# Kernel optimization log

Hardware: AMD Instinct MI355X
Metric: run time of the kernel (lower is better)

## Reference

```python
import jax, jax.numpy as jnp
import numpy as np

N = 200000          # number of points (dental scan vertices)
K = 16              # neighbors after dropping self (nsample=17 - 1)
C = 32              # feature dim (base_fdim)
NUM_CLASSES = 17
TEMPERATURE = 0.1
WEIGHT = 0.1        # head_cfg.weight[1:] of '.1'
EPS = 1e-8


def setup_inputs() -> dict:
    key = jax.random.key(0)
    k1, k2, k3 = jax.random.split(key, 3)
    features = jax.random.normal(k1, (N, C), dtype=jnp.float32)
    labels = jax.random.randint(k2, (N,), 0, NUM_CLASSES, dtype=jnp.int32)
    neighbor_idx = jax.random.randint(k3, (N, K), 0, N, dtype=jnp.int64)
    return {"features": features, "labels": labels, "neighbor_idx": neighbor_idx}


def reference(features, labels, neighbor_idx):
    # gather neighbor features/labels: [N, K, C] / [N, K]
    nb_feat = features[neighbor_idx]
    nb_lab = labels[neighbor_idx]

    # posmask_cnt: same class as center point (labels are argmaxed one-hots)
    posmask = nb_lab == labels[:, None]                     # [N, K] bool

    # point_mask: points with at least one positive and one negative neighbor
    cnt = jnp.sum(posmask.astype(jnp.int32), axis=-1)       # [N]
    point_mask = jnp.logical_and(cnt > 0, cnt < K)          # [N] bool

    # dist_l2
    diff = features[:, None, :] - nb_feat                   # [N, K, C]
    dist = jnp.sqrt(jnp.sum(diff * diff, axis=-1) + EPS)    # [N, K]

    # contrast_softnn (stable softmax over neighbors)
    d = -dist
    d = (d - jnp.max(d, axis=-1, keepdims=True)) / TEMPERATURE
    e = jnp.exp(d)                                          # [N, K]
    pos = jnp.sum(e * posmask.astype(e.dtype), axis=-1)
    neg = jnp.sum(e, axis=-1)
    loss = -jnp.log(pos / neg + EPS)                        # [N]

    # masked mean over valid points (== filtering before the mean)
    pm = point_mask.astype(loss.dtype)
    denom = jnp.maximum(jnp.sum(pm), 1.0)
    mean_loss = jnp.sum(loss * pm) / denom
    return mean_loss * WEIGHT
```

## Files before the change

### kernel.cpp

```cpp
#include <hip/hip_runtime.h>
#include <math.h>
#include <string.h>

#define NPTS 200000
#define KNBR 16
#define CDIM 32
#define NITEM (NPTS * KNBR)
#define TEMP 0.1f
#define WEIGHT 0.1f
#define EPSV 1e-8f

#define BLD_BLOCKS ((NPTS + 255) / 256)

#define PD_BLOCKS 1248
#define PD_RANKS 3125
#define PD_GSTRIDE 624

#define SMP_BLOCKS 625
#define SMP_ITER 5
#define SMP_STRIDE (SMP_BLOCKS * 1024)

#define QS 0.55f

#define TBLA_OFF 256
#define TBLB_OFF (TBLA_OFF + NPTS * 16)
#define D2A_OFF  (TBLB_OFF + NPTS * 16)
#define D2B_OFF  (D2A_OFF + NITEM * 2)
#define BL_OFF   (D2B_OFF + NITEM * 2)
#define BC_OFF   (BL_OFF + SMP_BLOCKS * 4)
#define WS_NEEDED ((size_t)(BC_OFF + SMP_BLOCKS * 4))

typedef float v2f __attribute__((ext_vector_type(2)));
typedef float v4f __attribute__((ext_vector_type(4)));
typedef int   v4i __attribute__((ext_vector_type(4)));
typedef unsigned v4u __attribute__((ext_vector_type(4)));
typedef unsigned v2u __attribute__((ext_vector_type(2)));

static __device__ __forceinline__ unsigned short f32_to_f16b(float x) {
    _Float16 h = (_Float16)x;
    unsigned short u;
    __builtin_memcpy(&u, &h, 2);
    return u;
}
static __device__ __forceinline__ float f16b_to_f32(unsigned short u) {
    _Float16 h;
    __builtin_memcpy(&h, &u, 2);
    return (float)h;
}
static __device__ __forceinline__ int q4(float x) {
    int q = (int)rintf(x * (1.0f / QS)) + 7;
    return q < 0 ? 0 : (q > 14 ? 14 : q);
}

__global__ __launch_bounds__(256) void build_tables(
    const float* __restrict__ f, const int* __restrict__ labels,
    unsigned char* __restrict__ A, unsigned char* __restrict__ B) {
    const int p = blockIdx.x * 256 + threadIdx.x;
    if (p >= NPTS) return;
    const v4f* fp = (const v4f*)(f + (size_t)p * CDIM);
    const v4f v0 = __builtin_nontemporal_load(fp + 0);
    const v4f v1 = __builtin_nontemporal_load(fp + 1);
    const v4f v2 = __builtin_nontemporal_load(fp + 2);
    const v4f v3 = __builtin_nontemporal_load(fp + 3);
    const v4f v4 = __builtin_nontemporal_load(fp + 4);
    const v4f v5 = __builtin_nontemporal_load(fp + 5);
    const v4f v6 = __builtin_nontemporal_load(fp + 6);
    const v4f v7 = __builtin_nontemporal_load(fp + 7);

    int a0 = 0, a1 = 0, a2 = 0, a3 = 0;
    a0 = __builtin_amdgcn_cvt_pk_fp8_f32(v0.x, v0.y, a0, false);
    a0 = __builtin_amdgcn_cvt_pk_fp8_f32(v0.z, v0.w, a0, true);
    a1 = __builtin_amdgcn_cvt_pk_fp8_f32(v1.x, v1.y, a1, false);
    a1 = __builtin_amdgcn_cvt_pk_fp8_f32(v1.z, v1.w, a1, true);
    a2 = __builtin_amdgcn_cvt_pk_fp8_f32(v2.x, v2.y, a2, false);
    a2 = __builtin_amdgcn_cvt_pk_fp8_f32(v2.z, v2.w, a2, true);
    a3 = __builtin_amdgcn_cvt_pk_fp8_f32(v3.x, v3.y, a3, false);
    a3 = __builtin_amdgcn_cvt_pk_fp8_f32(v3.z, v3.w, a3, true);
    v4u ra; ra.x = (unsigned)a0; ra.y = (unsigned)a1;
    ra.z = (unsigned)a2; ra.w = (unsigned)a3;
    *(v4u*)(A + (size_t)p * 16) = ra;

    int b0 = 0, b1 = 0, b2 = 0, b3 = 0;
    b0 = __builtin_amdgcn_cvt_pk_fp8_f32(v4.x, v4.y, b0, false);
    b0 = __builtin_amdgcn_cvt_pk_fp8_f32(v4.z, v4.w, b0, true);
    b1 = __builtin_amdgcn_cvt_pk_fp8_f32(v5.x, v5.y, b1, false);
    b1 = __builtin_amdgcn_cvt_pk_fp8_f32(v5.z, v5.w, b1, true);
    b2 = __builtin_amdgcn_cvt_pk_fp8_f32(v6.x, v6.y, b2, false);
    b2 = __builtin_amdgcn_cvt_pk_fp8_f32(v6.z, v6.w, b2, true);
    b3 = __builtin_amdgcn_cvt_pk_fp8_f32(v7.x, v7.y, b3, false);
    const int pk = q4(v7.z) | (q4(v7.w) << 4);
    b3 = (b3 & 0xffff) | (pk << 16) | ((labels[p] & 0xff) << 24);
    v4u rb; rb.x = (unsigned)b0; rb.y = (unsigned)b1;
    rb.z = (unsigned)b2; rb.w = (unsigned)b3;
    *(v4u*)(B + (size_t)p * 16) = rb;
}

__global__ __launch_bounds__(256) void partial_d2(
    const unsigned char* __restrict__ tblA,
    const unsigned char* __restrict__ tblB,
    const int* __restrict__ nbr,
    unsigned short* __restrict__ d2A,
    unsigned short* __restrict__ d2B) {
    const int b = blockIdx.x;
    const int grp = (b >> 2) & 1;
    const int r = (b >> 3) * 4 + (b & 3);
    const unsigned char* __restrict__ tbl = grp ? tblB : tblA;
    unsigned short* __restrict__ dst = grp ? d2B : d2A;

    for (int rr = r; rr < PD_RANKS; rr += PD_GSTRIDE) {
        const int i = rr * 1024 + threadIdx.x * 4;
        const v4i idx4 = __builtin_nontemporal_load((const v4i*)(nbr + i));
        const int p = i >> 4;
        const v4u cv = *(const v4u*)(tbl + (size_t)p * 16);

        v4u nv[4];
        nv[0] = *(const v4u*)(tbl + (size_t)idx4.x * 16);
        nv[1] = *(const v4u*)(tbl + (size_t)idx4.y * 16);
        nv[2] = *(const v4u*)(tbl + (size_t)idx4.z * 16);
        nv[3] = *(const v4u*)(tbl + (size_t)idx4.w * 16);

        unsigned short o[4];
        if (grp == 0) {
            v2f c[8];
            #pragma unroll
            for (int q = 0; q < 4; ++q) {
                c[2 * q]     = __builtin_amdgcn_cvt_pk_f32_fp8((int)cv[q], false);
                c[2 * q + 1] = __builtin_amdgcn_cvt_pk_f32_fp8((int)cv[q], true);
            }
            #pragma unroll
            for (int k = 0; k < 4; ++k) {
                float d2 = 0.f;
                #pragma unroll
                for (int q = 0; q < 4; ++q) {
                    v2f nl = __builtin_amdgcn_cvt_pk_f32_fp8((int)nv[k][q], false);
                    v2f nh = __builtin_amdgcn_cvt_pk_f32_fp8((int)nv[k][q], true);
                    float a0 = c[2 * q].x - nl.x, a1 = c[2 * q].y - nl.y;
                    float a2 = c[2 * q + 1].x - nh.x, a3 = c[2 * q + 1].y - nh.y;
                    d2 += a0 * a0 + a1 * a1 + a2 * a2 + a3 * a3;
                }
                o[k] = f32_to_f16b(d2);
            }
        } else {
            v2f c[7];
            #pragma unroll
            for (int q = 0; q < 3; ++q) {
                c[2 * q]     = __builtin_amdgcn_cvt_pk_f32_fp8((int)cv[q], false);
                c[2 * q + 1] = __builtin_amdgcn_cvt_pk_f32_fp8((int)cv[q], true);
            }
            c[6] = __builtin_amdgcn_cvt_pk_f32_fp8((int)cv[3], false);
            const unsigned cb = (cv[3] >> 16) & 0xffu;
            const float c30 = (float)(cb & 15u) * QS - 7.0f * QS;
            const float c31 = (float)(cb >> 4) * QS - 7.0f * QS;
            const unsigned clab = cv[3] >> 24;
            #pragma unroll
            for (int k = 0; k < 4; ++k) {
                float d2 = 0.f;
                #pragma unroll
                for (int q = 0; q < 3; ++q) {
                    v2f nl = __builtin_amdgcn_cvt_pk_f32_fp8((int)nv[k][q], false);
                    v2f nh = __builtin_amdgcn_cvt_pk_f32_fp8((int)nv[k][q], true);
                    float a0 = c[2 * q].x - nl.x, a1 = c[2 * q].y - nl.y;
                    float a2 = c[2 * q + 1].x - nh.x, a3 = c[2 * q + 1].y - nh.y;
                    d2 += a0 * a0 + a1 * a1 + a2 * a2 + a3 * a3;
                }
                {
                    v2f nl = __builtin_amdgcn_cvt_pk_f32_fp8((int)nv[k][3], false);
                    float a0 = c[6].x - nl.x, a1 = c[6].y - nl.y;
                    d2 += a0 * a0 + a1 * a1;
                }
                {
                    const unsigned nb = (nv[k][3] >> 16) & 0xffu;
                    const float n30 = (float)(nb & 15u) * QS - 7.0f * QS;
                    const float n31 = (float)(nb >> 4) * QS - 7.0f * QS;
                    const float a0 = c30 - n30, a1 = c31 - n31;
                    d2 += a0 * a0 + a1 * a1;
                }
                const bool pos = (nv[k][3] >> 24) == clab;
                o[k] = (unsigned short)(f32_to_f16b(d2) | (pos ? 0x8000u : 0u));
            }
        }
        v2u pk2;
        pk2.x = (unsigned)o[0] | ((unsigned)o[1] << 16);
        pk2.y = (unsigned)o[2] | ((unsigned)o[3] << 16);
        __builtin_nontemporal_store(pk2, (v2u*)(dst + i));
    }
}

__global__ __launch_bounds__(256) void softmax_part(
    const unsigned short* __restrict__ d2A,
    const unsigned short* __restrict__ d2B,
    float* __restrict__ bl, float* __restrict__ bc) {
    const int tid = threadIdx.x;
    const int lane = tid & 63;
    float loss_acc = 0.f, valid_acc = 0.f;

    for (int k = 0; k < SMP_ITER; ++k) {
        const int i = blockIdx.x * 1024 + tid * 4 + k * SMP_STRIDE;
        const v2u ua = __builtin_nontemporal_load((const v2u*)(d2A + i));
        const v2u ub = __builtin_nontemporal_load((const v2u*)(d2B + i));

        float d[4];
        bool pos[4];
        #pragma unroll
        for (int j = 0; j < 4; ++j) {
            const unsigned short a = (unsigned short)((j < 2 ? ua.x : ua.y) >> ((j & 1) * 16));
            const unsigned short bb = (unsigned short)((j < 2 ? ub.x : ub.y) >> ((j & 1) * 16));
            pos[j] = (bb & 0x8000u) != 0;
            d[j] = sqrtf(f16b_to_f32(a) + f16b_to_f32(bb & 0x7fffu) + EPSV);
        }

        float mn = fminf(fminf(d[0], d[1]), fminf(d[2], d[3]));
        mn = fminf(mn, __shfl_xor(mn, 1));
        mn = fminf(mn, __shfl_xor(mn, 2));

        float pos_s = 0.f, neg_s = 0.f, cnt_s = 0.f;
        #pragma unroll
        for (int j = 0; j < 4; ++j) {
            const float e = expf((mn - d[j]) * (1.0f / TEMP));
            neg_s += e;
            if (pos[j]) { pos_s += e; cnt_s += 1.f; }
        }
        #pragma unroll
        for (int off = 1; off <= 2; off <<= 1) {
            pos_s += __shfl_xor(pos_s, off);
            neg_s += __shfl_xor(neg_s, off);
            cnt_s += __shfl_xor(cnt_s, off);
        }
        if ((lane & 3) == 0) {
            const int icnt = (int)(cnt_s + 0.5f);
            if (icnt > 0 && icnt < KNBR) {
                loss_acc += -logf(pos_s / neg_s + EPSV);
                valid_acc += 1.f;
            }
        }
    }

    #pragma unroll
    for (int off = 4; off <= 32; off <<= 1) {
        loss_acc += __shfl_xor(loss_acc, off);
        valid_acc += __shfl_xor(valid_acc, off);
    }

    __shared__ float sl[4], sv[4];
    if (lane == 0) { sl[tid >> 6] = loss_acc; sv[tid >> 6] = valid_acc; }
    __syncthreads();
    if (tid == 0) {
        bl[blockIdx.x] = sl[0] + sl[1] + sl[2] + sl[3];
        bc[blockIdx.x] = sv[0] + sv[1] + sv[2] + sv[3];
    }
}

__global__ __launch_bounds__(256) void final_reduce(const float* __restrict__ bl,
                                                    const float* __restrict__ bc,
                                                    float* __restrict__ out) {
    const int tid = threadIdx.x;
    float l = 0.f, v = 0.f;
    for (int i = tid; i < SMP_BLOCKS; i += 256) { l += bl[i]; v += bc[i]; }
    #pragma unroll
    for (int off = 1; off <= 32; off <<= 1) {
        l += __shfl_xor(l, off);
        v += __shfl_xor(v, off);
    }
    __shared__ float sl[4], sv[4];
    if ((tid & 63) == 0) { sl[tid >> 6] = l; sv[tid >> 6] = v; }
    __syncthreads();
    if (tid == 0) {
        const float S = sl[0] + sl[1] + sl[2] + sl[3];
        const float C = sv[0] + sv[1] + sv[2] + sv[3];
        out[0] = S / fmaxf(C, 1.f) * WEIGHT;
    }
}

__global__ __launch_bounds__(256) void contrast_fp32(
    const float* __restrict__ features,
    const int* __restrict__ labels,
    const int* __restrict__ nbr,
    float* __restrict__ ws) {
    const int lane = threadIdx.x & 63;
    const int wave = threadIdx.x >> 6;
    const int p0 = blockIdx.x * 16 + wave * 4;
    const int m = lane >> 3;
    const int c = lane & 7;
    const int idx_l = nbr[p0 * KNBR + lane];
    const int labn_l = labels[idx_l];
    const int labc_l = labels[p0 + (lane >> 4)];
    float4 cen[4];
    #pragma unroll
    for (int pt = 0; pt < 4; ++pt)
        cen[pt] = *(const float4*)(features + (size_t)(p0 + pt) * CDIM + c * 4);
    int ridx[8];
    #pragma unroll
    for (int j = 0; j < 8; ++j) ridx[j] = __shfl(idx_l, 8 * j + m);
    float4 v[8];
    #pragma unroll
    for (int j = 0; j < 8; ++j)
        v[j] = *(const float4*)(features + (size_t)ridx[j] * CDIM + c * 4);
    float dj[8];
    #pragma unroll
    for (int j = 0; j < 8; ++j) {
        float4 ce = cen[j >> 1];
        float dx = ce.x - v[j].x, dy = ce.y - v[j].y;
        float dz = ce.z - v[j].z, dw = ce.w - v[j].w;
        float d2 = dx * dx + dy * dy + dz * dz + dw * dw;
        d2 += __shfl_xor(d2, 1);
        d2 += __shfl_xor(d2, 2);
        d2 += __shfl_xor(d2, 4);
        dj[j] = sqrtf(d2 + EPSV);
    }
    float loss_acc = 0.f, valid_acc = 0.f;
    #pragma unroll
    for (int pt = 0; pt < 4; ++pt) {
        float a = dj[2 * pt], b = dj[2 * pt + 1];
        float mn = fminf(a, b);
        mn = fminf(mn, __shfl_xor(mn, 8));
        mn = fminf(mn, __shfl_xor(mn, 16));
        mn = fminf(mn, __shfl_xor(mn, 32));
        const float ea = expf((mn - a) / TEMP);
        const float eb = expf((mn - b) / TEMP);
        const int la = __shfl(labn_l, 16 * pt + m);
        const int lb = __shfl(labn_l, 16 * pt + 8 + m);
        const int lc = __shfl(labc_l, 16 * pt);
        float pos_s = (la == lc ? ea : 0.f) + (lb == lc ? eb : 0.f);
        float neg_s = ea + eb;
        float cnt_s = (la == lc ? 1.f : 0.f) + (lb == lc ? 1.f : 0.f);
        #pragma unroll
        for (int off = 8; off <= 32; off <<= 1) {
            pos_s += __shfl_xor(pos_s, off);
            neg_s += __shfl_xor(neg_s, off);
            cnt_s += __shfl_xor(cnt_s, off);
        }
        if (lane == pt) {
            const int icnt = (int)(cnt_s + 0.5f);
            if (icnt > 0 && icnt < KNBR) {
                loss_acc += -logf(pos_s / neg_s + EPSV);
                valid_acc += 1.f;
            }
        }
    }
    __shared__ float s_loss, s_cnt;
    if (threadIdx.x == 0) { s_loss = 0.f; s_cnt = 0.f; }
    __syncthreads();
    if (lane < 4) { atomicAdd(&s_loss, loss_acc); atomicAdd(&s_cnt, valid_acc); }
    __syncthreads();
    if (threadIdx.x == 0) { atomicAdd(&ws[0], s_loss); atomicAdd(&ws[1], s_cnt); }
}

__global__ void contrast_finalize(const float* __restrict__ ws,
                                  float* __restrict__ out) {
    out[0] = ws[0] / fmaxf(ws[1], 1.f) * WEIGHT;
}

extern "C" void kernel_launch(void* const* d_in, const int* in_sizes, int n_in,
                              void* d_out, int out_size, void* d_ws, size_t ws_size,
                              hipStream_t stream) {
    const float* features = (const float*)d_in[0];
    const int* labels     = (const int*)d_in[1];
    const int* nbr        = (const int*)d_in[2];
    float* out = (float*)d_out;
    float* ws  = (float*)d_ws;

    if (ws_size >= WS_NEEDED) {
        unsigned char* tblA = (unsigned char*)d_ws + TBLA_OFF;
        unsigned char* tblB = (unsigned char*)d_ws + TBLB_OFF;
        unsigned short* d2A = (unsigned short*)((char*)d_ws + D2A_OFF);
        unsigned short* d2B = (unsigned short*)((char*)d_ws + D2B_OFF);
        float* bl = (float*)((char*)d_ws + BL_OFF);
        float* bc = (float*)((char*)d_ws + BC_OFF);

        build_tables<<<BLD_BLOCKS, 256, 0, stream>>>(features, labels, tblA, tblB);
        partial_d2<<<PD_BLOCKS, 256, 0, stream>>>(tblA, tblB, nbr, d2A, d2B);
        softmax_part<<<SMP_BLOCKS, 256, 0, stream>>>(d2A, d2B, bl, bc);
        final_reduce<<<1, 256, 0, stream>>>(bl, bc, out);
    } else {
        (void)hipMemsetAsync(ws, 0, 16, stream);
        contrast_fp32<<<NPTS / 16, 256, 0, stream>>>(features, labels, nbr, ws);
        contrast_finalize<<<1, 1, 0, stream>>>(ws, out);
    }
}
```

Measured before the change: 135.9 us.

## Fuse four-kernel pipeline into one cooperative kernel with grid syncs

Replaces the four separate launches (table build, partial distances, softmax, final reduce) with a single cooperative kernel of 1024 blocks that uses grid-wide syncs between the stages. The aim is to remove the launch gaps and inter-kernel drain between short stages. The cost is three grid barriers and a fixed grid size that may balance work less well. The build stage covers only 1024*256 points, which is enough for 200000. The old multi-kernel path is kept as a fallback if the cooperative launch fails.

```diff
diff --git a/kernel.cpp b/kernel.cpp
--- a/kernel.cpp
+++ b/kernel.cpp
@@ -1,21 +1,24 @@
 #include <hip/hip_runtime.h>
+#include <hip/hip_cooperative_groups.h>
 #include <math.h>
 #include <string.h>
+
+namespace cg = cooperative_groups;
 
 #define NPTS 200000
 #define KNBR 16
 #define CDIM 32
 #define NITEM (NPTS * KNBR)
+#define NCHUNK (NITEM / 1024)
 #define TEMP 0.1f
 #define WEIGHT 0.1f
 #define EPSV 1e-8f
 
+#define MEGA_GRID 1024
+
 #define BLD_BLOCKS ((NPTS + 255) / 256)
-
 #define PD_BLOCKS 1248
-#define PD_RANKS 3125
 #define PD_GSTRIDE 624
-
 #define SMP_BLOCKS 625
 #define SMP_ITER 5
 #define SMP_STRIDE (SMP_BLOCKS * 1024)
@@ -27,8 +30,8 @@
 #define D2A_OFF  (TBLB_OFF + NPTS * 16)
 #define D2B_OFF  (D2A_OFF + NITEM * 2)
 #define BL_OFF   (D2B_OFF + NITEM * 2)
-#define BC_OFF   (BL_OFF + SMP_BLOCKS * 4)
-#define WS_NEEDED ((size_t)(BC_OFF + SMP_BLOCKS * 4))
+#define BC_OFF   (BL_OFF + MEGA_GRID * 4)
+#define WS_NEEDED ((size_t)(BC_OFF + MEGA_GRID * 4))
 
 typedef float v2f __attribute__((ext_vector_type(2)));
 typedef float v4f __attribute__((ext_vector_type(4)));
@@ -52,11 +55,9 @@
     return q < 0 ? 0 : (q > 14 ? 14 : q);
 }
 
-__global__ __launch_bounds__(256) void build_tables(
-    const float* __restrict__ f, const int* __restrict__ labels,
+static __device__ __forceinline__ void build_one(
+    const float* __restrict__ f, const int* __restrict__ labels, int p,
     unsigned char* __restrict__ A, unsigned char* __restrict__ B) {
-    const int p = blockIdx.x * 256 + threadIdx.x;
-    if (p >= NPTS) return;
     const v4f* fp = (const v4f*)(f + (size_t)p * CDIM);
     const v4f v0 = __builtin_nontemporal_load(fp + 0);
     const v4f v1 = __builtin_nontemporal_load(fp + 1);
@@ -95,6 +96,200 @@
     *(v4u*)(B + (size_t)p * 16) = rb;
 }
 
+static __device__ __forceinline__ void pd2_chunk(
+    const unsigned char* __restrict__ tbl, const int* __restrict__ nbr,
+    unsigned short* __restrict__ dst, int grp, int i0, int tid) {
+    const int i = i0 + tid * 4;
+    const v4i idx4 = __builtin_nontemporal_load((const v4i*)(nbr + i));
+    const int p = i >> 4;
+    const v4u cv = *(const v4u*)(tbl + (size_t)p * 16);
+
+    v4u nv[4];
+    nv[0] = *(const v4u*)(tbl + (size_t)idx4.x * 16);
+    nv[1] = *(const v4u*)(tbl + (size_t)idx4.y * 16);
+    nv[2] = *(const v4u*)(tbl + (size_t)idx4.z * 16);
+    nv[3] = *(const v4u*)(tbl + (size_t)idx4.w * 16);
+
+    unsigned short o[4];
+    if (grp == 0) {
+        v2f c[8];
+        #pragma unroll
+        for (int q = 0; q < 4; ++q) {
+            c[2 * q]     = __builtin_amdgcn_cvt_pk_f32_fp8((int)cv[q], false);
+            c[2 * q + 1] = __builtin_amdgcn_cvt_pk_f32_fp8((int)cv[q], true);
+        }
+        #pragma unroll
+        for (int k = 0; k < 4; ++k) {
+            float d2 = 0.f;
+            #pragma unroll
+            for (int q = 0; q < 4; ++q) {
+                v2f nl = __builtin_amdgcn_cvt_pk_f32_fp8((int)nv[k][q], false);
+                v2f nh = __builtin_amdgcn_cvt_pk_f32_fp8((int)nv[k][q], true);
+                float a0 = c[2 * q].x - nl.x, a1 = c[2 * q].y - nl.y;
+                float a2 = c[2 * q + 1].x - nh.x, a3 = c[2 * q + 1].y - nh.y;
+                d2 += a0 * a0 + a1 * a1 + a2 * a2 + a3 * a3;
+            }
+            o[k] = f32_to_f16b(d2);
+        }
+    } else {
+        v2f c[7];
+        #pragma unroll
+        for (int q = 0; q < 3; ++q) {
+            c[2 * q]     = __builtin_amdgcn_cvt_pk_f32_fp8((int)cv[q], false);
+            c[2 * q + 1] = __builtin_amdgcn_cvt_pk_f32_fp8((int)cv[q], true);
+        }
+        c[6] = __builtin_amdgcn_cvt_pk_f32_fp8((int)cv[3], false);
+        const unsigned cb = (cv[3] >> 16) & 0xffu;
+        const float c30 = (float)(cb & 15u) * QS - 7.0f * QS;
+        const float c31 = (float)(cb >> 4) * QS - 7.0f * QS;
+        const unsigned clab = cv[3] >> 24;
+        #pragma unroll
+        for (int k = 0; k < 4; ++k) {
+            float d2 = 0.f;
+            #pragma unroll
+            for (int q = 0; q < 3; ++q) {
+                v2f nl = __builtin_amdgcn_cvt_pk_f32_fp8((int)nv[k][q], false);
+                v2f nh = __builtin_amdgcn_cvt_pk_f32_fp8((int)nv[k][q], true);
+                float a0 = c[2 * q].x - nl.x, a1 = c[2 * q].y - nl.y;
+                float a2 = c[2 * q + 1].x - nh.x, a3 = c[2 * q + 1].y - nh.y;
+                d2 += a0 * a0 + a1 * a1 + a2 * a2 + a3 * a3;
+            }
+            {
+                v2f nl = __builtin_amdgcn_cvt_pk_f32_fp8((int)nv[k][3], false);
+                float a0 = c[6].x - nl.x, a1 = c[6].y - nl.y;
+                d2 += a0 * a0 + a1 * a1;
+            }
+            {
+                const unsigned nb = (nv[k][3] >> 16) & 0xffu;
+                const float n30 = (float)(nb & 15u) * QS - 7.0f * QS;
+                const float n31 = (float)(nb >> 4) * QS - 7.0f * QS;
+                const float a0 = c30 - n30, a1 = c31 - n31;
+                d2 += a0 * a0 + a1 * a1;
+            }
+            const bool pos = (nv[k][3] >> 24) == clab;
+            o[k] = (unsigned short)(f32_to_f16b(d2) | (pos ? 0x8000u : 0u));
+        }
+    }
+    v2u pk2;
+    pk2.x = (unsigned)o[0] | ((unsigned)o[1] << 16);
+    pk2.y = (unsigned)o[2] | ((unsigned)o[3] << 16);
+    __builtin_nontemporal_store(pk2, (v2u*)(dst + i));
+}
+
+static __device__ __forceinline__ void sm_chunk(
+    const unsigned short* __restrict__ d2A, const unsigned short* __restrict__ d2B,
+    int i0, int tid, int lane, float& loss_acc, float& valid_acc) {
+    const int i = i0 + tid * 4;
+    const v2u ua = __builtin_nontemporal_load((const v2u*)(d2A + i));
+    const v2u ub = __builtin_nontemporal_load((const v2u*)(d2B + i));
+
+    float d[4];
+    bool pos[4];
+    #pragma unroll
+    for (int j = 0; j < 4; ++j) {
+        const unsigned short a = (unsigned short)((j < 2 ? ua.x : ua.y) >> ((j & 1) * 16));
+        const unsigned short bb = (unsigned short)((j < 2 ? ub.x : ub.y) >> ((j & 1) * 16));
+        pos[j] = (bb & 0x8000u) != 0;
+        d[j] = sqrtf(f16b_to_f32(a) + f16b_to_f32(bb & 0x7fffu) + EPSV);
+    }
+    float mn = fminf(fminf(d[0], d[1]), fminf(d[2], d[3]));
+    mn = fminf(mn, __shfl_xor(mn, 1));
+    mn = fminf(mn, __shfl_xor(mn, 2));
+
+    float pos_s = 0.f, neg_s = 0.f, cnt_s = 0.f;
+    #pragma unroll
+    for (int j = 0; j < 4; ++j) {
+        const float e = expf((mn - d[j]) * (1.0f / TEMP));
+        neg_s += e;
+        if (pos[j]) { pos_s += e; cnt_s += 1.f; }
+    }
+    #pragma unroll
+    for (int off = 1; off <= 2; off <<= 1) {
+        pos_s += __shfl_xor(pos_s, off);
+        neg_s += __shfl_xor(neg_s, off);
+        cnt_s += __shfl_xor(cnt_s, off);
+    }
+    if ((lane & 3) == 0) {
+        const int icnt = (int)(cnt_s + 0.5f);
+        if (icnt > 0 && icnt < KNBR) {
+            loss_acc += -logf(pos_s / neg_s + EPSV);
+            valid_acc += 1.f;
+        }
+    }
+}
+
+__global__ __launch_bounds__(256) void mega(
+    const float* __restrict__ f, const int* __restrict__ labels,
+    const int* __restrict__ nbr,
+    unsigned char* __restrict__ tblA, unsigned char* __restrict__ tblB,
+    unsigned short* __restrict__ d2A, unsigned short* __restrict__ d2B,
+    float* __restrict__ bl, float* __restrict__ bc, float* __restrict__ out) {
+    cg::grid_group grid = cg::this_grid();
+    const int tid = threadIdx.x;
+    const int bid = blockIdx.x;
+    const int lane = tid & 63;
+
+    {
+        const int p = bid * 256 + tid;
+        if (p < NPTS) build_one(f, labels, p, tblA, tblB);
+    }
+    grid.sync();
+
+    {
+        const int grp = ((bid & 7) < 4) ? 0 : 1;
+        const int r = (bid >> 3) * 4 + (bid & 3);
+        const unsigned char* tbl = grp ? tblB : tblA;
+        unsigned short* dst = grp ? d2B : d2A;
+        for (int c = r; c < NCHUNK; c += 512)
+            pd2_chunk(tbl, nbr, dst, grp, c * 1024, tid);
+    }
+    grid.sync();
+
+    {
+        float loss_acc = 0.f, valid_acc = 0.f;
+        for (int c = bid; c < NCHUNK; c += MEGA_GRID)
+            sm_chunk(d2A, d2B, c * 1024, tid, lane, loss_acc, valid_acc);
+        #pragma unroll
+        for (int off = 4; off <= 32; off <<= 1) {
+            loss_acc += __shfl_xor(loss_acc, off);
+            valid_acc += __shfl_xor(valid_acc, off);
+        }
+        __shared__ float sl[4], sv[4];
+        if (lane == 0) { sl[tid >> 6] = loss_acc; sv[tid >> 6] = valid_acc; }
+        __syncthreads();
+        if (tid == 0) {
+            bl[bid] = sl[0] + sl[1] + sl[2] + sl[3];
+            bc[bid] = sv[0] + sv[1] + sv[2] + sv[3];
+        }
+    }
+    grid.sync();
+
+    if (bid == 0) {
+        float l = 0.f, v = 0.f;
+        for (int i = tid; i < MEGA_GRID; i += 256) { l += bl[i]; v += bc[i]; }
+        #pragma unroll
+        for (int off = 1; off <= 32; off <<= 1) {
+            l += __shfl_xor(l, off);
+            v += __shfl_xor(v, off);
+        }
+        __shared__ float sl2[4], sv2[4];
+        if ((tid & 63) == 0) { sl2[tid >> 6] = l; sv2[tid >> 6] = v; }
+        __syncthreads();
+        if (tid == 0) {
+            const float S = sl2[0] + sl2[1] + sl2[2] + sl2[3];
+            const float C = sv2[0] + sv2[1] + sv2[2] + sv2[3];
+            out[0] = S / fmaxf(C, 1.f) * WEIGHT;
+        }
+    }
+}
+
+__global__ __launch_bounds__(256) void build_tables(
+    const float* __restrict__ f, const int* __restrict__ labels,
+    unsigned char* __restrict__ A, unsigned char* __restrict__ B) {
+    const int p = blockIdx.x * 256 + threadIdx.x;
+    if (p < NPTS) build_one(f, labels, p, A, B);
+}
+
 __global__ __launch_bounds__(256) void partial_d2(
     const unsigned char* __restrict__ tblA,
     const unsigned char* __restrict__ tblB,
@@ -104,86 +299,10 @@
     const int b = blockIdx.x;
     const int grp = (b >> 2) & 1;
     const int r = (b >> 3) * 4 + (b & 3);
-    const unsigned char* __restrict__ tbl = grp ? tblB : tblA;
-    unsigned short* __restrict__ dst = grp ? d2B : d2A;
-
-    for (int rr = r; rr < PD_RANKS; rr += PD_GSTRIDE) {
-        const int i = rr * 1024 + threadIdx.x * 4;
-        const v4i idx4 = __builtin_nontemporal_load((const v4i*)(nbr + i));
-        const int p = i >> 4;
-        const v4u cv = *(const v4u*)(tbl + (size_t)p * 16);
-
-        v4u nv[4];
-        nv[0] = *(const v4u*)(tbl + (size_t)idx4.x * 16);
-        nv[1] = *(const v4u*)(tbl + (size_t)idx4.y * 16);
-        nv[2] = *(const v4u*)(tbl + (size_t)idx4.z * 16);
-        nv[3] = *(const v4u*)(tbl + (size_t)idx4.w * 16);
-
-        unsigned short o[4];
-        if (grp == 0) {
-            v2f c[8];
-            #pragma unroll
-            for (int q = 0; q < 4; ++q) {
-                c[2 * q]     = __builtin_amdgcn_cvt_pk_f32_fp8((int)cv[q], false);
-                c[2 * q + 1] = __builtin_amdgcn_cvt_pk_f32_fp8((int)cv[q], true);
-            }
-            #pragma unroll
-            for (int k = 0; k < 4; ++k) {
-                float d2 = 0.f;
-                #pragma unroll
-                for (int q = 0; q < 4; ++q) {
-                    v2f nl = __builtin_amdgcn_cvt_pk_f32_fp8((int)nv[k][q], false);
-                    v2f nh = __builtin_amdgcn_cvt_pk_f32_fp8((int)nv[k][q], true);
-                    float a0 = c[2 * q].x - nl.x, a1 = c[2 * q].y - nl.y;
-                    float a2 = c[2 * q + 1].x - nh.x, a3 = c[2 * q + 1].y - nh.y;
-                    d2 += a0 * a0 + a1 * a1 + a2 * a2 + a3 * a3;
-                }
-                o[k] = f32_to_f16b(d2);
-            }
-        } else {
-            v2f c[7];
-            #pragma unroll
-            for (int q = 0; q < 3; ++q) {
-                c[2 * q]     = __builtin_amdgcn_cvt_pk_f32_fp8((int)cv[q], false);
-                c[2 * q + 1] = __builtin_amdgcn_cvt_pk_f32_fp8((int)cv[q], true);
-            }
-            c[6] = __builtin_amdgcn_cvt_pk_f32_fp8((int)cv[3], false);
-            const unsigned cb = (cv[3] >> 16) & 0xffu;
-            const float c30 = (float)(cb & 15u) * QS - 7.0f * QS;
-            const float c31 = (float)(cb >> 4) * QS - 7.0f * QS;
-            const unsigned clab = cv[3] >> 24;
-            #pragma unroll
-            for (int k = 0; k < 4; ++k) {
-                float d2 = 0.f;
-                #pragma unroll
-                for (int q = 0; q < 3; ++q) {
-                    v2f nl = __builtin_amdgcn_cvt_pk_f32_fp8((int)nv[k][q], false);
-                    v2f nh = __builtin_amdgcn_cvt_pk_f32_fp8((int)nv[k][q], true);
-                    float a0 = c[2 * q].x - nl.x, a1 = c[2 * q].y - nl.y;
-                    float a2 = c[2 * q + 1].x - nh.x, a3 = c[2 * q + 1].y - nh.y;
-                    d2 += a0 * a0 + a1 * a1 + a2 * a2 + a3 * a3;
-                }
-                {
-                    v2f nl = __builtin_amdgcn_cvt_pk_f32_fp8((int)nv[k][3], false);
-                    float a0 = c[6].x - nl.x, a1 = c[6].y - nl.y;
-                    d2 += a0 * a0 + a1 * a1;
-                }
-                {
-                    const unsigned nb = (nv[k][3] >> 16) & 0xffu;
-                    const float n30 = (float)(nb & 15u) * QS - 7.0f * QS;
-                    const float n31 = (float)(nb >> 4) * QS - 7.0f * QS;
-                    const float a0 = c30 - n30, a1 = c31 - n31;
-                    d2 += a0 * a0 + a1 * a1;
-                }
-                const bool pos = (nv[k][3] >> 24) == clab;
-                o[k] = (unsigned short)(f32_to_f16b(d2) | (pos ? 0x8000u : 0u));
-            }
-        }
-        v2u pk2;
-        pk2.x = (unsigned)o[0] | ((unsigned)o[1] << 16);
-        pk2.y = (unsigned)o[2] | ((unsigned)o[3] << 16);
-        __builtin_nontemporal_store(pk2, (v2u*)(dst + i));
-    }
+    const unsigned char* tbl = grp ? tblB : tblA;
+    unsigned short* dst = grp ? d2B : d2A;
+    for (int rr = r; rr < NCHUNK; rr += PD_GSTRIDE)
+        pd2_chunk(tbl, nbr, dst, grp, rr * 1024, threadIdx.x);
 }
 
 __global__ __launch_bounds__(256) void softmax_part(
@@ -193,54 +312,14 @@
     const int tid = threadIdx.x;
     const int lane = tid & 63;
     float loss_acc = 0.f, valid_acc = 0.f;
-
-    for (int k = 0; k < SMP_ITER; ++k) {
-        const int i = blockIdx.x * 1024 + tid * 4 + k * SMP_STRIDE;
-        const v2u ua = __builtin_nontemporal_load((const v2u*)(d2A + i));
-        const v2u ub = __builtin_nontemporal_load((const v2u*)(d2B + i));
-
-        float d[4];
-        bool pos[4];
-        #pragma unroll
-        for (int j = 0; j < 4; ++j) {
-            const unsigned short a = (unsigned short)((j < 2 ? ua.x : ua.y) >> ((j & 1) * 16));
-            const unsigned short bb = (unsigned short)((j < 2 ? ub.x : ub.y) >> ((j & 1) * 16));
-            pos[j] = (bb & 0x8000u) != 0;
-            d[j] = sqrtf(f16b_to_f32(a) + f16b_to_f32(bb & 0x7fffu) + EPSV);
-        }
-
-        float mn = fminf(fminf(d[0], d[1]), fminf(d[2], d[3]));
-        mn = fminf(mn, __shfl_xor(mn, 1));
-        mn = fminf(mn, __shfl_xor(mn, 2));
-
-        float pos_s = 0.f, neg_s = 0.f, cnt_s = 0.f;
-        #pragma unroll
-        for (int j = 0; j < 4; ++j) {
-            const float e = expf((mn - d[j]) * (1.0f / TEMP));
-            neg_s += e;
-            if (pos[j]) { pos_s += e; cnt_s += 1.f; }
-        }
-        #pragma unroll
-        for (int off = 1; off <= 2; off <<= 1) {
-            pos_s += __shfl_xor(pos_s, off);
-            neg_s += __shfl_xor(neg_s, off);
-            cnt_s += __shfl_xor(cnt_s, off);
-        }
-        if ((lane & 3) == 0) {
-            const int icnt = (int)(cnt_s + 0.5f);
-            if (icnt > 0 && icnt < KNBR) {
-                loss_acc += -logf(pos_s / neg_s + EPSV);
-                valid_acc += 1.f;
-            }
-        }
-    }
-
+    for (int k = 0; k < SMP_ITER; ++k)
+        sm_chunk(d2A, d2B, blockIdx.x * 1024 + k * SMP_STRIDE, tid, lane,
+                 loss_acc, valid_acc);
     #pragma unroll
     for (int off = 4; off <= 32; off <<= 1) {
         loss_acc += __shfl_xor(loss_acc, off);
         valid_acc += __shfl_xor(valid_acc, off);
     }
-
     __shared__ float sl[4], sv[4];
     if (lane == 0) { sl[tid >> 6] = loss_acc; sv[tid >> 6] = valid_acc; }
     __syncthreads();
@@ -252,10 +331,11 @@
 
 __global__ __launch_bounds__(256) void final_reduce(const float* __restrict__ bl,
                                                     const float* __restrict__ bc,
-                                                    float* __restrict__ out) {
+                                                    float* __restrict__ out,
+                                                    int n) {
     const int tid = threadIdx.x;
     float l = 0.f, v = 0.f;
-    for (int i = tid; i < SMP_BLOCKS; i += 256) { l += bl[i]; v += bc[i]; }
+    for (int i = tid; i < n; i += 256) { l += bl[i]; v += bc[i]; }
     #pragma unroll
     for (int off = 1; off <= 32; off <<= 1) {
         l += __shfl_xor(l, off);
@@ -367,10 +447,18 @@
         float* bl = (float*)((char*)d_ws + BL_OFF);
         float* bc = (float*)((char*)d_ws + BC_OFF);
 
-        build_tables<<<BLD_BLOCKS, 256, 0, stream>>>(features, labels, tblA, tblB);
-        partial_d2<<<PD_BLOCKS, 256, 0, stream>>>(tblA, tblB, nbr, d2A, d2B);
-        softmax_part<<<SMP_BLOCKS, 256, 0, stream>>>(d2A, d2B, bl, bc);
-        final_reduce<<<1, 256, 0, stream>>>(bl, bc, out);
+        void* args[] = {(void*)&features, (void*)&labels, (void*)&nbr,
+                        (void*)&tblA, (void*)&tblB, (void*)&d2A, (void*)&d2B,
+                        (void*)&bl, (void*)&bc, (void*)&out};
+        hipError_t e = hipLaunchCooperativeKernel((const void*)mega,
+                                                  dim3(MEGA_GRID), dim3(256),
+                                                  args, 0, stream);
+        if (e != hipSuccess) {
+            build_tables<<<BLD_BLOCKS, 256, 0, stream>>>(features, labels, tblA, tblB);
+            partial_d2<<<PD_BLOCKS, 256, 0, stream>>>(tblA, tblB, nbr, d2A, d2B);
+            softmax_part<<<SMP_BLOCKS, 256, 0, stream>>>(d2A, d2B, bl, bc);
+            final_reduce<<<1, 256, 0, stream>>>(bl, bc, out, SMP_BLOCKS);
+        }
     } else {
         (void)hipMemsetAsync(ws, 0, 16, stream);
         contrast_fp32<<<NPTS / 16, 256, 0, stream>>>(features, labels, nbr, ws);
```

After: 489.3 us. 260% more time.
